# Kernel optimization log

Measured on AMD Instinct MI355X. Metric: run time of the kernel, lower is better.

The kernel has to match this reference:

```python
import jax, jax.numpy as jnp
import numpy as np

D_MODEL = 1024
NUM_HEADS = 16
DEPTH = D_MODEL // NUM_HEADS


def setup_inputs() -> dict:
    key = jax.random.key(0)
    ks = jax.random.split(key, 9)
    B, S = 2, 2048
    s = 1.0 / np.sqrt(D_MODEL)
    return {
        "x": jax.random.normal(ks[0], (B, S, D_MODEL), dtype=jnp.float32),
        "wq": jax.random.normal(ks[1], (D_MODEL, D_MODEL), dtype=jnp.float32) * s,
        "bq": jnp.zeros((D_MODEL,), dtype=jnp.float32),
        "wk": jax.random.normal(ks[2], (D_MODEL, D_MODEL), dtype=jnp.float32) * s,
        "bk": jnp.zeros((D_MODEL,), dtype=jnp.float32),
        "wv": jax.random.normal(ks[3], (D_MODEL, D_MODEL), dtype=jnp.float32) * s,
        "bv": jnp.zeros((D_MODEL,), dtype=jnp.float32),
        "wo": jax.random.normal(ks[4], (D_MODEL, D_MODEL), dtype=jnp.float32) * s,
        "bo": jnp.zeros((D_MODEL,), dtype=jnp.float32),
    }


def _split_heads(t):
    # [B, S, D] -> [B, H, S, depth]
    B, S, _ = t.shape
    return t.reshape(B, S, NUM_HEADS, DEPTH).transpose(0, 2, 1, 3)


def reference(x, wq, bq, wk, bk, wv, bv, wo, bo):
    B, S, _ = x.shape
    q = _split_heads(x @ wq + bq)
    k = _split_heads(x @ wk + bk)
    v = _split_heads(x @ wv + bv)
    scale = 1.0 / jnp.sqrt(jnp.asarray(DEPTH, dtype=x.dtype))
    logits = jnp.einsum("bhsd,bhtd->bhst", q, k) * scale  # [B,H,S,S]
    attn = jax.nn.softmax(logits, axis=-1)
    ctx = jnp.einsum("bhst,bhtd->bhsd", attn, v)  # [B,H,S,depth]
    concat = ctx.transpose(0, 2, 1, 3).reshape(B, S, D_MODEL)
    return concat @ wo + bo
```

## Files before the change

### kernel.cpp

```cpp
#include <hip/hip_runtime.h>
#include <hip/hip_bf16.h>

typedef __bf16 bf16;
typedef __bf16 bf16x4 __attribute__((ext_vector_type(4)));
typedef __bf16 bf16x8 __attribute__((ext_vector_type(8)));
typedef float f32x4 __attribute__((ext_vector_type(4)));

typedef __attribute__((address_space(3))) void lds_void;
typedef const __attribute__((address_space(1))) void gbl_void;

#define D_MODEL 1024
#define NHEAD 16
#define DEPTH 64
#define SEQ 2048
#define BATCH 2
#define NTOK (BATCH * SEQ)

#define Q_SCALE 0.18033688f

__global__ __launch_bounds__(256) void prep(const float* __restrict__ w0,
                                            const float* __restrict__ w1,
                                            const float* __restrict__ w2,
                                            const float* __restrict__ w3,
                                            const float* __restrict__ x,
                                            bf16* __restrict__ wtb,
                                            bf16* __restrict__ xb) {
    int z = blockIdx.z;
    int tx = threadIdx.x, ty = threadIdx.y;
    if (z < 4) {
        const float* w = (z == 0) ? w0 : (z == 1) ? w1 : (z == 2) ? w2 : w3;
        bf16* d = wtb + (size_t)z * D_MODEL * D_MODEL;
        __shared__ float tile[32][33];
        int c0 = blockIdx.x * 32;
        int r0 = blockIdx.y * 32;
#pragma unroll
        for (int i = 0; i < 4; i++)
            tile[ty + i * 8][tx] = w[(size_t)(r0 + ty + i * 8) * D_MODEL + c0 + tx];
        __syncthreads();
#pragma unroll
        for (int i = 0; i < 4; i++)
            d[(size_t)(c0 + ty + i * 8) * D_MODEL + r0 + tx] = (bf16)tile[tx][ty + i * 8];
    } else {
        int t = ty * 32 + tx;
        size_t i = ((size_t)(z - 4) * 1024 + blockIdx.y * 32 + blockIdx.x) * 256 + t;
        float4 v = ((const float4*)x)[i];
        bf16x4 o = {(bf16)v.x, (bf16)v.y, (bf16)v.z, (bf16)v.w};
        *(bf16x4*)&xb[i * 4] = o;
    }
}

__global__ __launch_bounds__(512, 2) void qkv_gemm(const bf16* __restrict__ xb,
                                                   const bf16* __restrict__ wtb,
                                                   const float* __restrict__ bq,
                                                   const float* __restrict__ bk,
                                                   const float* __restrict__ bv,
                                                   bf16* __restrict__ q,
                                                   bf16* __restrict__ k,
                                                   bf16* __restrict__ v) {
    __shared__ bf16 sm[65536];

    const int flat = blockIdx.x;
    const int wg = (flat & 7) * 24 + (flat >> 3);
    const int mt = wg & 15, nt = wg >> 4;
    const int row0 = mt << 8;
    const int z = nt >> 2;
    const int nb = (nt & 3) << 8;

    const int tid = threadIdx.x;
    const int lane = tid & 63, wave = tid >> 6;
    const int wm = wave >> 2, wn = wave & 3;
    const int quad = lane >> 4, l16 = lane & 15;
    const int kch = ((quad ^ ((l16 >> 1) & 3)) << 3);

    const int srow = lane >> 2;
    const int scg = (lane & 3) ^ ((lane >> 3) & 3);
    const int stDst = wave * 1024 + lane * 8;

    const bf16* Ag = xb + (size_t)(row0 + wave * 32 + srow) * D_MODEL + scg * 8;
    const bf16* Bg = wtb + (size_t)z * D_MODEL * D_MODEL
                   + (size_t)(nb + wave * 32 + srow) * D_MODEL + scg * 8;

    f32x4 acc[8][4] = {};
    bf16x8 bfr[4];

#define GLL(SRC, DST) __builtin_amdgcn_global_load_lds((gbl_void*)(SRC), (lds_void*)(DST), 16, 0, 0)
#define STG_A(T_, KQ_, BUF_) { \
    const bf16* s_ = Ag + (T_) * 64 + (KQ_) * 32; \
    bf16* d_ = sm + (BUF_) * 16384 + (KQ_) * 8192 + stDst; \
    GLL(s_, d_); GLL(s_ + 16 * D_MODEL, d_ + 512); }
#define STG_B(T_, KQ_, BUF_) { \
    const bf16* s_ = Bg + (T_) * 64 + (KQ_) * 32; \
    bf16* d_ = sm + 32768 + (BUF_) * 16384 + (KQ_) * 8192 + stDst; \
    GLL(s_, d_); GLL(s_ + 16 * D_MODEL, d_ + 512); }
#define WAIT6 { asm volatile("s_waitcnt vmcnt(6)" ::: "memory"); }
#define NOW

#define PHASE(BUF_, KQ_, MQ_, STG_STMT, WAIT_STMT) { \
    bf16x8 af[4]; \
    const int ab_ = (BUF_) * 16384 + (KQ_) * 8192 + (wm * 128 + (MQ_) * 64 + l16) * 32 + kch; \
    _Pragma("unroll") \
    for (int i_ = 0; i_ < 4; i_++) af[i_] = *(const bf16x8*)&sm[ab_ + i_ * 512]; \
    if ((MQ_) == 0) { \
        const int bb_ = 32768 + (BUF_) * 16384 + (KQ_) * 8192 + (wn * 64 + l16) * 32 + kch; \
        _Pragma("unroll") \
        for (int j_ = 0; j_ < 4; j_++) bfr[j_] = *(const bf16x8*)&sm[bb_ + j_ * 512]; \
    } \
    STG_STMT; \
    WAIT_STMT; \
    __builtin_amdgcn_sched_barrier(0); \
    __builtin_amdgcn_s_barrier(); \
    __builtin_amdgcn_s_setprio(1); \
    _Pragma("unroll") \
    for (int i_ = 0; i_ < 4; i_++) \
        _Pragma("unroll") \
        for (int j_ = 0; j_ < 4; j_++) \
            acc[(MQ_) * 4 + i_][j_] = __builtin_amdgcn_mfma_f32_16x16x32_bf16( \
                af[i_], bfr[j_], acc[(MQ_) * 4 + i_][j_], 0, 0, 0); \
    __builtin_amdgcn_s_setprio(0); \
    __builtin_amdgcn_sched_barrier(0); \
    __builtin_amdgcn_s_barrier(); }

    STG_B(0, 0, 0);
    STG_A(0, 0, 0);
    STG_B(0, 1, 0);
    STG_A(0, 1, 0);
    asm volatile("s_waitcnt vmcnt(4)" ::: "memory");
    STG_B(1, 0, 1);
    STG_A(1, 0, 1);
    STG_B(1, 1, 1);
    asm volatile("s_waitcnt vmcnt(6)" ::: "memory");
    __builtin_amdgcn_sched_barrier(0);
    __builtin_amdgcn_s_barrier();

#pragma unroll 1
    for (int it = 0; it < 8; ++it) {
        const int t1 = 2 * it + 1;
        const int t2 = (2 * it + 2) & 15;
        const int t3 = (2 * it + 3) & 15;
        PHASE(0, 0, 0, STG_A(t1, 1, 1), NOW)
        PHASE(0, 0, 1, STG_B(t2, 0, 0), NOW)
        PHASE(0, 1, 0, STG_A(t2, 0, 0), NOW)
        PHASE(0, 1, 1, STG_B(t2, 1, 0), WAIT6)
        PHASE(1, 0, 0, STG_A(t2, 1, 0), NOW)
        PHASE(1, 0, 1, STG_B(t3, 0, 1), NOW)
        PHASE(1, 1, 0, STG_A(t3, 0, 1), NOW)
        PHASE(1, 1, 1, STG_B(t3, 1, 1), WAIT6)
    }

#undef PHASE
#undef WAIT6
#undef NOW
#undef STG_A
#undef STG_B
#undef GLL

    const float* bias = (z == 0) ? bq : (z == 1) ? bk : bv;
    const int bI = row0 >> 11;
    const int sBase = row0 & 2047;
    if (z < 2) {
        bf16* dst = (z == 0) ? q : k;
        const float scl = (z == 0) ? Q_SCALE : 1.0f;
#pragma unroll
        for (int j = 0; j < 4; j++) {
            const int f = nb + wn * 64 + j * 16 + l16;
            const float bi = bias[f];
            const int hh = f >> 6, d = f & 63;
            bf16* dcol = dst + ((size_t)(bI * NHEAD + hh) * SEQ) * DEPTH + d;
#pragma unroll
            for (int mi = 0; mi < 8; mi++) {
                const int s0 = sBase + wm * 128 + (mi >> 2) * 64 + (mi & 3) * 16 + quad * 4;
#pragma unroll
                for (int r = 0; r < 4; r++)
                    dcol[(size_t)(s0 + r) * DEPTH] = (bf16)((acc[mi][j][r] + bi) * scl);
            }
        }
    } else {
#pragma unroll
        for (int j = 0; j < 4; j++) {
            const int f = nb + wn * 64 + j * 16 + l16;
            const float bi = bias[f];
            const int hh = f >> 6, d = f & 63;
            bf16* vrow = v + ((size_t)(bI * NHEAD + hh) * DEPTH + d) * SEQ;
#pragma unroll
            for (int mi = 0; mi < 8; mi++) {
                const int s0 = sBase + wm * 128 + (mi >> 2) * 64 + (mi & 3) * 16 + quad * 4;
                f32x4 a = acc[mi][j];
                bf16x4 ob = {(bf16)(a[0] + bi), (bf16)(a[1] + bi),
                             (bf16)(a[2] + bi), (bf16)(a[3] + bi)};
                *(bf16x4*)&vrow[s0] = ob;
            }
        }
    }
}

__global__ __launch_bounds__(256) void attn(const bf16* __restrict__ q,
                                            const bf16* __restrict__ k,
                                            const bf16* __restrict__ v,
                                            bf16* __restrict__ ctx) {
    __shared__ bf16 Ks[64 * 72];
    __shared__ bf16 Vs[64 * 72];
    __shared__ bf16 Ps[4][32 * 72];
    const int tid = threadIdx.x;
    const int lane = tid & 63, wave = tid >> 6;
    const int quad = lane >> 4, l16 = lane & 15;
    const int bh = blockIdx.x;
    const int q0 = blockIdx.y * 128;
    const size_t hb = (size_t)bh * SEQ * DEPTH;
    const bf16* qh = q + hb;
    const bf16* kh = k + hb;
    const bf16* vh = v + hb;

    bf16x8 bq_[2][2];
#pragma unroll
    for (int g = 0; g < 2; g++) {
        int qrow = q0 + wave * 32 + g * 16 + l16;
#pragma unroll
        for (int c = 0; c < 2; c++)
            bq_[g][c] = *(const bf16x8*)&qh[(size_t)qrow * DEPTH + c * 32 + quad * 8];
    }
    bf16* myP = &Ps[wave][0];

    bf16x8 ones;
#pragma unroll
    for (int i = 0; i < 8; i++) ones[i] = (bf16)1.0f;

    f32x4 ov[2][4] = {};
    f32x4 lacc[2] = {};

    const int srow = tid >> 2, scol = (tid & 3) << 4;
    const bf16* kg = kh + (size_t)srow * DEPTH + scol;
    const bf16* vg = vh + (size_t)srow * SEQ + scol;
    bf16* ksd = &Ks[srow * 72 + scol];
    bf16* vsd = &Vs[srow * 72 + scol];

    bf16x8 kr0 = *(const bf16x8*)kg, kr1 = *(const bf16x8*)(kg + 8);
    bf16x8 vr0 = *(const bf16x8*)vg, vr1 = *(const bf16x8*)(vg + 8);

    for (int t0 = 0; t0 < SEQ; t0 += 64) {
        __syncthreads();
        *(bf16x8*)ksd = kr0;  *(bf16x8*)(ksd + 8) = kr1;
        *(bf16x8*)vsd = vr0;  *(bf16x8*)(vsd + 8) = vr1;
        __syncthreads();
        if (t0 + 64 < SEQ) {
            const bf16* kgn = kg + (size_t)(t0 + 64) * DEPTH;
            const bf16* vgn = vg + (t0 + 64);
            kr0 = *(const bf16x8*)kgn;  kr1 = *(const bf16x8*)(kgn + 8);
            vr0 = *(const bf16x8*)vgn;  vr1 = *(const bf16x8*)(vgn + 8);
        }
        f32x4 sc[2][4] = {};
#pragma unroll
        for (int c = 0; c < 2; c++)
#pragma unroll
            for (int j = 0; j < 4; j++) {
                bf16x8 kf = *(const bf16x8*)&Ks[(j * 16 + l16) * 72 + c * 32 + quad * 8];
#pragma unroll
                for (int g = 0; g < 2; g++)
                    sc[g][j] = __builtin_amdgcn_mfma_f32_16x16x32_bf16(kf, bq_[g][c], sc[g][j], 0, 0, 0);
            }
#pragma unroll
        for (int g = 0; g < 2; g++)
#pragma unroll
            for (int j = 0; j < 4; j++) {
                bf16x4 pb = {(bf16)__builtin_amdgcn_exp2f(sc[g][j][0]),
                             (bf16)__builtin_amdgcn_exp2f(sc[g][j][1]),
                             (bf16)__builtin_amdgcn_exp2f(sc[g][j][2]),
                             (bf16)__builtin_amdgcn_exp2f(sc[g][j][3])};
                *(bf16x4*)&myP[(g * 16 + l16) * 72 + j * 16 + quad * 4] = pb;
            }
#pragma unroll
        for (int c = 0; c < 2; c++) {
            bf16x8 pf[2];
#pragma unroll
            for (int g = 0; g < 2; g++) {
                pf[g] = *(const bf16x8*)&myP[(g * 16 + l16) * 72 + c * 32 + quad * 8];
                lacc[g] = __builtin_amdgcn_mfma_f32_16x16x32_bf16(ones, pf[g], lacc[g], 0, 0, 0);
            }
#pragma unroll
            for (int t = 0; t < 4; t++) {
                bf16x8 vf = *(const bf16x8*)&Vs[(t * 16 + l16) * 72 + c * 32 + quad * 8];
#pragma unroll
                for (int g = 0; g < 2; g++)
                    ov[g][t] = __builtin_amdgcn_mfma_f32_16x16x32_bf16(vf, pf[g], ov[g][t], 0, 0, 0);
            }
        }
    }
    int b = bh >> 4, hh = bh & 15;
#pragma unroll
    for (int g = 0; g < 2; g++) {
        float inv = 1.0f / lacc[g][0];
        size_t rowb = ((size_t)(b * SEQ + q0 + wave * 32 + g * 16 + l16)) * D_MODEL + hh * 64;
#pragma unroll
        for (int t = 0; t < 4; t++) {
            bf16x4 ob = {(bf16)(ov[g][t][0] * inv), (bf16)(ov[g][t][1] * inv),
                         (bf16)(ov[g][t][2] * inv), (bf16)(ov[g][t][3] * inv)};
            *(bf16x4*)&ctx[rowb + t * 16 + quad * 4] = ob;
        }
    }
}

__global__ __launch_bounds__(256) void out_gemm(const bf16* __restrict__ ctx,
                                                const bf16* __restrict__ wot,
                                                const float* __restrict__ bo,
                                                float* __restrict__ out) {
    __shared__ bf16 As[64 * 32];
    __shared__ bf16 Bs[128 * 32];
    const int tid = threadIdx.x;
    const int lane = tid & 63, wave = tid >> 6;
    const int quad = lane >> 4, l16 = lane & 15;
    const int srow = lane >> 2, selem = (lane & 3) * 8;
    int row0 = blockIdx.y * 64, col0 = blockIdx.x * 128;
    f32x4 acc[4][2] = {};

    for (int k0 = 0; k0 < D_MODEL; k0 += 32) {
        __syncthreads();
        {
            const bf16* ga = ctx + (size_t)(row0 + wave * 16 + srow) * D_MODEL + k0 + selem;
            __builtin_amdgcn_global_load_lds((gbl_void*)ga, (lds_void*)(As + wave * 512 + lane * 8), 16, 0, 0);
        }
#pragma unroll
        for (int t = 0; t < 2; t++) {
            int m = wave * 2 + t;
            const bf16* gb = wot + (size_t)(col0 + m * 16 + srow) * D_MODEL + k0 + selem;
            __builtin_amdgcn_global_load_lds((gbl_void*)gb, (lds_void*)(Bs + m * 512 + lane * 8), 16, 0, 0);
        }
        __syncthreads();
        bf16x8 af[4], bfr[2];
#pragma unroll
        for (int i = 0; i < 4; i++)
            af[i] = *(const bf16x8*)&As[(i * 16 + l16) * 32 + quad * 8];
#pragma unroll
        for (int j = 0; j < 2; j++)
            bfr[j] = *(const bf16x8*)&Bs[(wave * 32 + j * 16 + l16) * 32 + quad * 8];
#pragma unroll
        for (int i = 0; i < 4; i++)
#pragma unroll
            for (int j = 0; j < 2; j++)
                acc[i][j] = __builtin_amdgcn_mfma_f32_16x16x32_bf16(af[i], bfr[j], acc[i][j], 0, 0, 0);
    }
#pragma unroll
    for (int i = 0; i < 4; i++)
#pragma unroll
        for (int j = 0; j < 2; j++) {
            int colg = col0 + wave * 32 + j * 16 + l16;
            float bi = bo[colg];
            int rbase = row0 + i * 16 + quad * 4;
#pragma unroll
            for (int r = 0; r < 4; r++)
                out[(size_t)(rbase + r) * D_MODEL + colg] = acc[i][j][r] + bi;
        }
}

extern "C" void kernel_launch(void* const* d_in, const int* in_sizes, int n_in,
                              void* d_out, int out_size, void* d_ws, size_t ws_size,
                              hipStream_t stream) {
    const float* x  = (const float*)d_in[0];
    const float* wq = (const float*)d_in[1];
    const float* bq = (const float*)d_in[2];
    const float* wk = (const float*)d_in[3];
    const float* bk = (const float*)d_in[4];
    const float* wv = (const float*)d_in[5];
    const float* bv = (const float*)d_in[6];
    const float* wo = (const float*)d_in[7];
    const float* bo = (const float*)d_in[8];
    float* out = (float*)d_out;

    const size_t MB = 1024 * 1024;
    char* ws = (char*)d_ws;
    bf16* xb  = (bf16*)(ws);
    bf16* wtb = (bf16*)(ws + 8 * MB);
    bf16* qb  = (bf16*)(ws + 16 * MB);
    bf16* kb  = (bf16*)(ws + 24 * MB);
    bf16* vb  = (bf16*)(ws + 32 * MB);
    bf16* ctx = (bf16*)(ws + 40 * MB);

    prep<<<dim3(32, 32, 8), dim3(32, 8), 0, stream>>>(wq, wk, wv, wo, x, wtb, xb);
    qkv_gemm<<<dim3(192), dim3(512), 0, stream>>>(xb, wtb, bq, bk, bv, qb, kb, vb);
    attn<<<dim3(BATCH * NHEAD, SEQ / 128), 256, 0, stream>>>(qb, kb, vb, ctx);
    out_gemm<<<dim3(8, 64), 256, 0, stream>>>(ctx, wtb + 3 * (size_t)D_MODEL * D_MODEL, bo, out);
}
```

Measured before the change: 193.2 us.

## Halve attention query tile per block and XOR-swizzle LDS tiles

The attention kernel now gives each block 64 query rows, one 16-row group per wave, instead of 128 rows. The grid doubles along the sequence axis to expose more parallelism across CUs. The padded stride-72 shared-memory layouts for K, V and P are replaced by dense stride-64 layouts with an XOR swizzle on 8-element chunks, meant to avoid bank conflicts while using less LDS. The trade-off is that each K/V tile loaded into LDS is reused by half as many query rows, which doubles K/V global traffic and gives fewer MFMAs per LDS fragment read.

```diff
diff --git a/kernel.cpp b/kernel.cpp
--- a/kernel.cpp
+++ b/kernel.cpp
@@ -197,26 +197,26 @@
                                             const bf16* __restrict__ k,
                                             const bf16* __restrict__ v,
                                             bf16* __restrict__ ctx) {
-    __shared__ bf16 Ks[64 * 72];
-    __shared__ bf16 Vs[64 * 72];
-    __shared__ bf16 Ps[4][32 * 72];
+    __shared__ bf16 Ks[64 * 64];
+    __shared__ bf16 Vs[64 * 64];
+    __shared__ bf16 Ps[4][16 * 64];
     const int tid = threadIdx.x;
     const int lane = tid & 63, wave = tid >> 6;
     const int quad = lane >> 4, l16 = lane & 15;
+    const int m7 = l16 & 7;
     const int bh = blockIdx.x;
-    const int q0 = blockIdx.y * 128;
+    const int q0 = blockIdx.y * 64;
     const size_t hb = (size_t)bh * SEQ * DEPTH;
     const bf16* qh = q + hb;
     const bf16* kh = k + hb;
     const bf16* vh = v + hb;
 
-    bf16x8 bq_[2][2];
-#pragma unroll
-    for (int g = 0; g < 2; g++) {
-        int qrow = q0 + wave * 32 + g * 16 + l16;
+    bf16x8 bq_[2];
+    {
+        int qrow = q0 + wave * 16 + l16;
 #pragma unroll
         for (int c = 0; c < 2; c++)
-            bq_[g][c] = *(const bf16x8*)&qh[(size_t)qrow * DEPTH + c * 32 + quad * 8];
+            bq_[c] = *(const bf16x8*)&qh[(size_t)qrow * DEPTH + c * 32 + quad * 8];
     }
     bf16* myP = &Ps[wave][0];
 
@@ -224,22 +224,24 @@
 #pragma unroll
     for (int i = 0; i < 8; i++) ones[i] = (bf16)1.0f;
 
-    f32x4 ov[2][4] = {};
-    f32x4 lacc[2] = {};
-
-    const int srow = tid >> 2, scol = (tid & 3) << 4;
-    const bf16* kg = kh + (size_t)srow * DEPTH + scol;
-    const bf16* vg = vh + (size_t)srow * SEQ + scol;
-    bf16* ksd = &Ks[srow * 72 + scol];
-    bf16* vsd = &Vs[srow * 72 + scol];
+    f32x4 ov[4] = {};
+    f32x4 lacc = {};
+
+    const int srow = tid >> 2, ch0 = (tid & 3) * 2, sm7 = srow & 7;
+    const bf16* kg = kh + (size_t)srow * DEPTH + ch0 * 8;
+    const bf16* vg = vh + (size_t)srow * SEQ + ch0 * 8;
+    bf16* ksd0 = &Ks[srow * 64 + ((ch0)     ^ sm7) * 8];
+    bf16* ksd1 = &Ks[srow * 64 + ((ch0 + 1) ^ sm7) * 8];
+    bf16* vsd0 = &Vs[srow * 64 + ((ch0)     ^ sm7) * 8];
+    bf16* vsd1 = &Vs[srow * 64 + ((ch0 + 1) ^ sm7) * 8];
 
     bf16x8 kr0 = *(const bf16x8*)kg, kr1 = *(const bf16x8*)(kg + 8);
     bf16x8 vr0 = *(const bf16x8*)vg, vr1 = *(const bf16x8*)(vg + 8);
 
     for (int t0 = 0; t0 < SEQ; t0 += 64) {
         __syncthreads();
-        *(bf16x8*)ksd = kr0;  *(bf16x8*)(ksd + 8) = kr1;
-        *(bf16x8*)vsd = vr0;  *(bf16x8*)(vsd + 8) = vr1;
+        *(bf16x8*)ksd0 = kr0;  *(bf16x8*)ksd1 = kr1;
+        *(bf16x8*)vsd0 = vr0;  *(bf16x8*)vsd1 = vr1;
         __syncthreads();
         if (t0 + 64 < SEQ) {
             const bf16* kgn = kg + (size_t)(t0 + 64) * DEPTH;
@@ -247,54 +249,44 @@
             kr0 = *(const bf16x8*)kgn;  kr1 = *(const bf16x8*)(kgn + 8);
             vr0 = *(const bf16x8*)vgn;  vr1 = *(const bf16x8*)(vgn + 8);
         }
-        f32x4 sc[2][4] = {};
+        f32x4 sc[4] = {};
 #pragma unroll
         for (int c = 0; c < 2; c++)
 #pragma unroll
             for (int j = 0; j < 4; j++) {
-                bf16x8 kf = *(const bf16x8*)&Ks[(j * 16 + l16) * 72 + c * 32 + quad * 8];
-#pragma unroll
-                for (int g = 0; g < 2; g++)
-                    sc[g][j] = __builtin_amdgcn_mfma_f32_16x16x32_bf16(kf, bq_[g][c], sc[g][j], 0, 0, 0);
+                bf16x8 kf = *(const bf16x8*)&Ks[(j * 16 + l16) * 64 +
+                                                ((((c << 2) | quad) ^ m7) << 3)];
+                sc[j] = __builtin_amdgcn_mfma_f32_16x16x32_bf16(kf, bq_[c], sc[j], 0, 0, 0);
             }
 #pragma unroll
-        for (int g = 0; g < 2; g++)
-#pragma unroll
-            for (int j = 0; j < 4; j++) {
-                bf16x4 pb = {(bf16)__builtin_amdgcn_exp2f(sc[g][j][0]),
-                             (bf16)__builtin_amdgcn_exp2f(sc[g][j][1]),
-                             (bf16)__builtin_amdgcn_exp2f(sc[g][j][2]),
-                             (bf16)__builtin_amdgcn_exp2f(sc[g][j][3])};
-                *(bf16x4*)&myP[(g * 16 + l16) * 72 + j * 16 + quad * 4] = pb;
+        for (int j = 0; j < 4; j++) {
+            bf16x4 pb = {(bf16)__builtin_amdgcn_exp2f(sc[j][0]),
+                         (bf16)__builtin_amdgcn_exp2f(sc[j][1]),
+                         (bf16)__builtin_amdgcn_exp2f(sc[j][2]),
+                         (bf16)__builtin_amdgcn_exp2f(sc[j][3])};
+            int pos = (2 * j + (quad >> 1)) ^ m7;
+            *(bf16x4*)&myP[l16 * 64 + pos * 8 + (quad & 1) * 4] = pb;
+        }
+#pragma unroll
+        for (int c = 0; c < 2; c++) {
+            bf16x8 pf = *(const bf16x8*)&myP[l16 * 64 + ((((c << 2) | quad) ^ m7) << 3)];
+            lacc = __builtin_amdgcn_mfma_f32_16x16x32_bf16(ones, pf, lacc, 0, 0, 0);
+#pragma unroll
+            for (int t = 0; t < 4; t++) {
+                bf16x8 vf = *(const bf16x8*)&Vs[(t * 16 + l16) * 64 +
+                                                ((((c << 2) | quad) ^ m7) << 3)];
+                ov[t] = __builtin_amdgcn_mfma_f32_16x16x32_bf16(vf, pf, ov[t], 0, 0, 0);
             }
-#pragma unroll
-        for (int c = 0; c < 2; c++) {
-            bf16x8 pf[2];
-#pragma unroll
-            for (int g = 0; g < 2; g++) {
-                pf[g] = *(const bf16x8*)&myP[(g * 16 + l16) * 72 + c * 32 + quad * 8];
-                lacc[g] = __builtin_amdgcn_mfma_f32_16x16x32_bf16(ones, pf[g], lacc[g], 0, 0, 0);
-            }
-#pragma unroll
-            for (int t = 0; t < 4; t++) {
-                bf16x8 vf = *(const bf16x8*)&Vs[(t * 16 + l16) * 72 + c * 32 + quad * 8];
-#pragma unroll
-                for (int g = 0; g < 2; g++)
-                    ov[g][t] = __builtin_amdgcn_mfma_f32_16x16x32_bf16(vf, pf[g], ov[g][t], 0, 0, 0);
-            }
         }
     }
     int b = bh >> 4, hh = bh & 15;
-#pragma unroll
-    for (int g = 0; g < 2; g++) {
-        float inv = 1.0f / lacc[g][0];
-        size_t rowb = ((size_t)(b * SEQ + q0 + wave * 32 + g * 16 + l16)) * D_MODEL + hh * 64;
-#pragma unroll
-        for (int t = 0; t < 4; t++) {
-            bf16x4 ob = {(bf16)(ov[g][t][0] * inv), (bf16)(ov[g][t][1] * inv),
-                         (bf16)(ov[g][t][2] * inv), (bf16)(ov[g][t][3] * inv)};
-            *(bf16x4*)&ctx[rowb + t * 16 + quad * 4] = ob;
-        }
+    float inv = 1.0f / lacc[0];
+    size_t rowb = ((size_t)(b * SEQ + q0 + wave * 16 + l16)) * D_MODEL + hh * 64;
+#pragma unroll
+    for (int t = 0; t < 4; t++) {
+        bf16x4 ob = {(bf16)(ov[t][0] * inv), (bf16)(ov[t][1] * inv),
+                     (bf16)(ov[t][2] * inv), (bf16)(ov[t][3] * inv)};
+        *(bf16x4*)&ctx[rowb + t * 16 + quad * 4] = ob;
     }
 }
 
@@ -375,6 +367,6 @@
 
     prep<<<dim3(32, 32, 8), dim3(32, 8), 0, stream>>>(wq, wk, wv, wo, x, wtb, xb);
     qkv_gemm<<<dim3(192), dim3(512), 0, stream>>>(xb, wtb, bq, bk, bv, qb, kb, vb);
-    attn<<<dim3(BATCH * NHEAD, SEQ / 128), 256, 0, stream>>>(qb, kb, vb, ctx);
+    attn<<<dim3(BATCH * NHEAD, SEQ / 64), 256, 0, stream>>>(qb, kb, vb, ctx);
     out_gemm<<<dim3(8, 64), 256, 0, stream>>>(ctx, wtb + 3 * (size_t)D_MODEL * D_MODEL, bo, out);
 }
```

Measured after the change: 194.7 us. About the same (+0.8%).

## Split attention keys across waves with register-resident P and LDS reduction

Applied to the files above, without the earlier changes.

Restructures the attention kernel so each block handles 64 queries and the four waves split each 128-key tile among themselves, instead of each wave owning its own query rows. Probabilities stay in registers and feed the PV MFMA directly, and the row sum is accumulated in VALU, which removes the LDS round trip for P and the ones-MFMA. K/V tiles are loaded with global_load_lds into XOR-swizzled LDS, and a cross-wave LDS reduction combines the partial outputs and sums at the end. This doubles the grid size but drops the register prefetch double buffering, so each iteration now waits on its loads, and it adds an epilogue reduction.

```diff
diff --git a/kernel.cpp b/kernel.cpp
--- a/kernel.cpp
+++ b/kernel.cpp
@@ -197,104 +197,141 @@
                                             const bf16* __restrict__ k,
                                             const bf16* __restrict__ v,
                                             bf16* __restrict__ ctx) {
-    __shared__ bf16 Ks[64 * 72];
-    __shared__ bf16 Vs[64 * 72];
-    __shared__ bf16 Ps[4][32 * 72];
+    __shared__ __align__(16) char smem[36864];
+    bf16* Ks = (bf16*)smem;
+    bf16* Vs = (bf16*)(smem + 16384);
     const int tid = threadIdx.x;
     const int lane = tid & 63, wave = tid >> 6;
     const int quad = lane >> 4, l16 = lane & 15;
     const int bh = blockIdx.x;
-    const int q0 = blockIdx.y * 128;
+    const int q0 = blockIdx.y * 64;
     const size_t hb = (size_t)bh * SEQ * DEPTH;
     const bf16* qh = q + hb;
     const bf16* kh = k + hb;
     const bf16* vh = v + hb;
 
-    bf16x8 bq_[2][2];
-#pragma unroll
-    for (int g = 0; g < 2; g++) {
-        int qrow = q0 + wave * 32 + g * 16 + l16;
+    bf16x8 bq_[4][2];
+#pragma unroll
+    for (int n = 0; n < 4; n++) {
+        int qrow = q0 + n * 16 + l16;
 #pragma unroll
         for (int c = 0; c < 2; c++)
-            bq_[g][c] = *(const bf16x8*)&qh[(size_t)qrow * DEPTH + c * 32 + quad * 8];
-    }
-    bf16* myP = &Ps[wave][0];
-
-    bf16x8 ones;
-#pragma unroll
-    for (int i = 0; i < 8; i++) ones[i] = (bf16)1.0f;
-
-    f32x4 ov[2][4] = {};
-    f32x4 lacc[2] = {};
-
-    const int srow = tid >> 2, scol = (tid & 3) << 4;
-    const bf16* kg = kh + (size_t)srow * DEPTH + scol;
-    const bf16* vg = vh + (size_t)srow * SEQ + scol;
-    bf16* ksd = &Ks[srow * 72 + scol];
-    bf16* vsd = &Vs[srow * 72 + scol];
-
-    bf16x8 kr0 = *(const bf16x8*)kg, kr1 = *(const bf16x8*)(kg + 8);
-    bf16x8 vr0 = *(const bf16x8*)vg, vr1 = *(const bf16x8*)(vg + 8);
-
-    for (int t0 = 0; t0 < SEQ; t0 += 64) {
+            bq_[n][c] = *(const bf16x8*)&qh[(size_t)qrow * DEPTH + c * 32 + quad * 8];
+    }
+
+    f32x4 ov[4][4] = {};
+    f32x4 lv = {};
+
+    const int krow = wave * 32 + (lane >> 3);
+    const int kchS = (lane & 7) ^ (((lane >> 3) & 3) << 1);
+    const int vrow = wave * 16 + (lane >> 4);
+    const int krdRow = wave * 32 + ((l16 >> 2) << 3) + (l16 & 3);
+    const int ksw = ((l16 & 3) << 1) | ((l16 >> 2) & 1);
+    const int vrd = (((wave << 2) | quad) ^ l16) << 3;
+
+#define GLL(SRC, DST) __builtin_amdgcn_global_load_lds((gbl_void*)(SRC), (lds_void*)(DST), 16, 0, 0)
+
+#pragma unroll 1
+    for (int t0 = 0; t0 < SEQ; t0 += 128) {
         __syncthreads();
-        *(bf16x8*)ksd = kr0;  *(bf16x8*)(ksd + 8) = kr1;
-        *(bf16x8*)vsd = vr0;  *(bf16x8*)(vsd + 8) = vr1;
+#pragma unroll
+        for (int o = 0; o < 4; o++) {
+            const bf16* src = kh + (size_t)(t0 + krow + o * 8) * DEPTH
+                            + ((kchS ^ (o & 1)) << 3);
+            GLL(src, Ks + (wave * 32 + o * 8) * 64 + lane * 8);
+        }
+#pragma unroll
+        for (int o = 0; o < 4; o++) {
+            int rv = vrow + o * 4;
+            const bf16* src = vh + (size_t)rv * SEQ + t0
+                            + (((lane & 15) ^ (rv & 15)) << 3);
+            GLL(src, Vs + (wave * 16 + o * 4) * 128 + lane * 8);
+        }
         __syncthreads();
-        if (t0 + 64 < SEQ) {
-            const bf16* kgn = kg + (size_t)(t0 + 64) * DEPTH;
-            const bf16* vgn = vg + (t0 + 64);
-            kr0 = *(const bf16x8*)kgn;  kr1 = *(const bf16x8*)(kgn + 8);
-            vr0 = *(const bf16x8*)vgn;  vr1 = *(const bf16x8*)(vgn + 8);
-        }
-        f32x4 sc[2][4] = {};
+        f32x4 s[2][4] = {};
 #pragma unroll
         for (int c = 0; c < 2; c++)
 #pragma unroll
-            for (int j = 0; j < 4; j++) {
-                bf16x8 kf = *(const bf16x8*)&Ks[(j * 16 + l16) * 72 + c * 32 + quad * 8];
-#pragma unroll
-                for (int g = 0; g < 2; g++)
-                    sc[g][j] = __builtin_amdgcn_mfma_f32_16x16x32_bf16(kf, bq_[g][c], sc[g][j], 0, 0, 0);
+            for (int h = 0; h < 2; h++) {
+                bf16x8 kf = *(const bf16x8*)&Ks[(krdRow + h * 4) * 64 +
+                                                ((((c << 2) | quad) ^ ksw) << 3)];
+#pragma unroll
+                for (int n = 0; n < 4; n++)
+                    s[h][n] = __builtin_amdgcn_mfma_f32_16x16x32_bf16(kf, bq_[n][c], s[h][n], 0, 0, 0);
             }
-#pragma unroll
-        for (int g = 0; g < 2; g++)
-#pragma unroll
-            for (int j = 0; j < 4; j++) {
-                bf16x4 pb = {(bf16)__builtin_amdgcn_exp2f(sc[g][j][0]),
-                             (bf16)__builtin_amdgcn_exp2f(sc[g][j][1]),
-                             (bf16)__builtin_amdgcn_exp2f(sc[g][j][2]),
-                             (bf16)__builtin_amdgcn_exp2f(sc[g][j][3])};
-                *(bf16x4*)&myP[(g * 16 + l16) * 72 + j * 16 + quad * 4] = pb;
+        bf16x8 pb[4];
+#pragma unroll
+        for (int n = 0; n < 4; n++) {
+#pragma unroll
+            for (int h = 0; h < 2; h++) {
+                float e0 = __builtin_amdgcn_exp2f(s[h][n][0]);
+                float e1 = __builtin_amdgcn_exp2f(s[h][n][1]);
+                float e2 = __builtin_amdgcn_exp2f(s[h][n][2]);
+                float e3 = __builtin_amdgcn_exp2f(s[h][n][3]);
+                pb[n][h * 4 + 0] = (bf16)e0;
+                pb[n][h * 4 + 1] = (bf16)e1;
+                pb[n][h * 4 + 2] = (bf16)e2;
+                pb[n][h * 4 + 3] = (bf16)e3;
+                lv[n] += (e0 + e1) + (e2 + e3);
             }
-#pragma unroll
-        for (int c = 0; c < 2; c++) {
-            bf16x8 pf[2];
-#pragma unroll
-            for (int g = 0; g < 2; g++) {
-                pf[g] = *(const bf16x8*)&myP[(g * 16 + l16) * 72 + c * 32 + quad * 8];
-                lacc[g] = __builtin_amdgcn_mfma_f32_16x16x32_bf16(ones, pf[g], lacc[g], 0, 0, 0);
-            }
-#pragma unroll
-            for (int t = 0; t < 4; t++) {
-                bf16x8 vf = *(const bf16x8*)&Vs[(t * 16 + l16) * 72 + c * 32 + quad * 8];
-#pragma unroll
-                for (int g = 0; g < 2; g++)
-                    ov[g][t] = __builtin_amdgcn_mfma_f32_16x16x32_bf16(vf, pf[g], ov[g][t], 0, 0, 0);
-            }
-        }
-    }
-    int b = bh >> 4, hh = bh & 15;
-#pragma unroll
-    for (int g = 0; g < 2; g++) {
-        float inv = 1.0f / lacc[g][0];
-        size_t rowb = ((size_t)(b * SEQ + q0 + wave * 32 + g * 16 + l16)) * D_MODEL + hh * 64;
+        }
 #pragma unroll
         for (int t = 0; t < 4; t++) {
-            bf16x4 ob = {(bf16)(ov[g][t][0] * inv), (bf16)(ov[g][t][1] * inv),
-                         (bf16)(ov[g][t][2] * inv), (bf16)(ov[g][t][3] * inv)};
-            *(bf16x4*)&ctx[rowb + t * 16 + quad * 4] = ob;
-        }
+            bf16x8 vf = *(const bf16x8*)&Vs[(t * 16 + l16) * 128 + vrd];
+#pragma unroll
+            for (int n = 0; n < 4; n++)
+                ov[t][n] = __builtin_amdgcn_mfma_f32_16x16x32_bf16(vf, pb[n], ov[t][n], 0, 0, 0);
+        }
+    }
+#undef GLL
+
+    f32x4* Red  = (f32x4*)smem;
+    f32x4* Lred = (f32x4*)(smem + 32768);
+    __syncthreads();
+#pragma unroll
+    for (int tt = 0; tt < 8; tt++)
+        Red[(tt * 4 + wave) * 64 + lane] = ov[tt >> 2][tt & 3];
+    Lred[wave * 64 + lane] = lv;
+    __syncthreads();
+    f32x4 ls = {};
+#pragma unroll
+    for (int w_ = 0; w_ < 4; w_++)
+#pragma unroll
+        for (int qd = 0; qd < 4; qd++)
+            ls += Lred[w_ * 64 + qd * 16 + l16];
+    const int b = bh >> 4, hh = bh & 15;
+    const int wb1 = wave & 1;
+#pragma unroll
+    for (int u = 0; u < 2; u++) {
+        int tt = wave * 2 + u;
+        f32x4 sv = Red[(tt * 4 + 0) * 64 + lane] + Red[(tt * 4 + 1) * 64 + lane]
+                 + Red[(tt * 4 + 2) * 64 + lane] + Red[(tt * 4 + 3) * 64 + lane];
+        int n = wb1 * 2 + u, t = wave >> 1;
+        float iv = 1.0f / (wb1 ? ls[2 + u] : ls[u]);
+        bf16x4 ob = {(bf16)(sv[0] * iv), (bf16)(sv[1] * iv),
+                     (bf16)(sv[2] * iv), (bf16)(sv[3] * iv)};
+        size_t off = ((size_t)(b * SEQ + q0 + n * 16 + l16)) * D_MODEL
+                   + hh * 64 + t * 16 + quad * 4;
+        *(bf16x4*)&ctx[off] = ob;
+    }
+    __syncthreads();
+#pragma unroll
+    for (int tt = 8; tt < 16; tt++)
+        Red[((tt - 8) * 4 + wave) * 64 + lane] = ov[tt >> 2][tt & 3];
+    __syncthreads();
+#pragma unroll
+    for (int u = 0; u < 2; u++) {
+        int tt = 8 + wave * 2 + u;
+        int rt = tt - 8;
+        f32x4 sv = Red[(rt * 4 + 0) * 64 + lane] + Red[(rt * 4 + 1) * 64 + lane]
+                 + Red[(rt * 4 + 2) * 64 + lane] + Red[(rt * 4 + 3) * 64 + lane];
+        int n = wb1 * 2 + u, t = 2 + (wave >> 1);
+        float iv = 1.0f / (wb1 ? ls[2 + u] : ls[u]);
+        bf16x4 ob = {(bf16)(sv[0] * iv), (bf16)(sv[1] * iv),
+                     (bf16)(sv[2] * iv), (bf16)(sv[3] * iv)};
+        size_t off = ((size_t)(b * SEQ + q0 + n * 16 + l16)) * D_MODEL
+                   + hh * 64 + t * 16 + quad * 4;
+        *(bf16x4*)&ctx[off] = ob;
     }
 }
 
@@ -375,6 +412,6 @@
 
     prep<<<dim3(32, 32, 8), dim3(32, 8), 0, stream>>>(wq, wk, wv, wo, x, wtb, xb);
     qkv_gemm<<<dim3(192), dim3(512), 0, stream>>>(xb, wtb, bq, bk, bv, qb, kb, vb);
-    attn<<<dim3(BATCH * NHEAD, SEQ / 128), 256, 0, stream>>>(qb, kb, vb, ctx);
+    attn<<<dim3(BATCH * NHEAD, SEQ / 64), 256, 0, stream>>>(qb, kb, vb, ctx);
     out_gemm<<<dim3(8, 64), 256, 0, stream>>>(ctx, wtb + 3 * (size_t)D_MODEL * D_MODEL, bo, out);
 }
```

New measurement: 200.9 us. +4.0%, slower.
